# Optimization experiments

Hardware: AMD Instinct MI355X
Metric: run time of the kernel (lower is better)

Reference implementation:

```python
import jax, jax.numpy as jnp
import numpy as np

N_NODES = 50000
N_EDGES = 300000
H = 256
LN_EPS = 1e-5
NEG_SLOPE = 0.2  # PyG GATConv default


def layer_norm(x, g, b):
    mu = x.mean(-1, keepdims=True)
    var = ((x - mu) ** 2).mean(-1, keepdims=True)
    return (x - mu) * jax.lax.rsqrt(var + LN_EPS) * g + b


def gat_conv(x, src, dst, mask, W, a_src, a_dst, bias):
    # PyG GATConv(heads=1, concat=False) on the edge subset selected by `mask`,
    # with self-loops added for every node (PyG default add_self_loops=True).
    N = x.shape[0]
    h = x @ W                              # [N,H]
    s = h @ a_src                          # [N] alpha_src per node
    d = h @ a_dst                          # [N] alpha_dst per node
    e = jax.nn.leaky_relu(s[src] + d[dst], NEG_SLOPE)    # [E]
    e_masked = jnp.where(mask, e, -1e30)
    e_self = jax.nn.leaky_relu(s + d, NEG_SLOPE)         # [N] self-loop logits
    m = jnp.maximum(jax.ops.segment_max(e_masked, dst, num_segments=N), e_self)
    w = jnp.where(mask, jnp.exp(e - m[dst]), 0.0)        # masked edges -> 0
    w_self = jnp.exp(e_self - m)
    denom = jax.ops.segment_sum(w, dst, num_segments=N) + w_self
    num = jax.ops.segment_sum(w[:, None] * h[src], dst, num_segments=N) + w_self[:, None] * h
    return num / denom[:, None] + bias


def setup_inputs() -> dict:
    key = jax.random.key(0)
    ks = jax.random.split(key, 20)
    sc = 1.0 / np.sqrt(H)
    inp = {
        "x": jax.random.normal(ks[0], (N_NODES, H), jnp.float32),
        "edge_index": jax.random.randint(ks[1], (2, N_EDGES), 0, N_NODES, jnp.int64),
        "edge_attr": jax.random.randint(ks[2], (N_EDGES,), 0, 4, jnp.int64),
        # per-branch GATConv params (branches 0..2)
        "Wg": jax.random.normal(ks[3], (3, H, H), jnp.float32) * sc,
        "a_src": jax.random.normal(ks[4], (3, H), jnp.float32) * sc,
        "a_dst": jax.random.normal(ks[5], (3, H), jnp.float32) * sc,
        "bg": jnp.zeros((3, H), jnp.float32),
        # per-branch slice-strategy MLP: Linear + LayerNorm (+ReLU)
        "Ws": jax.random.normal(ks[6], (4, H, H), jnp.float32) * sc,
        "bs": jnp.zeros((4, H), jnp.float32),
        "gs": jnp.ones((4, H), jnp.float32),
        "betas": jnp.zeros((4, H), jnp.float32),
        # strategy selector MLP
        "W1": jax.random.normal(ks[7], (H, H // 2), jnp.float32) * sc,
        "b1": jnp.zeros((H // 2,), jnp.float32),
        "W2": jax.random.normal(ks[8], (H // 2, 4), jnp.float32) * (1.0 / np.sqrt(H // 2)),
        "b2": jnp.zeros((4,), jnp.float32),
        # fusion block
        "Wf": jax.random.normal(ks[9], (H, H), jnp.float32) * sc,
        "bf": jnp.zeros((H,), jnp.float32),
        "gf": jnp.ones((H,), jnp.float32),
        "betaf": jnp.zeros((H,), jnp.float32),
    }
    return inp


def reference(x, edge_index, edge_attr, Wg, a_src, a_dst, bg, Ws, bs, gs, betas,
              W1, b1, W2, b2, Wf, bf, gf, betaf):
    # strategy weights from mean graph representation (eval mode: dropout = identity)
    g = x.mean(axis=0)
    sw = jax.nn.softmax(jax.nn.relu(g @ W1 + b1) @ W2 + b2)  # [4]
    src, dst = edge_index[0], edge_index[1]
    combined = jnp.zeros_like(x)
    for i in range(4):
        if i < 3:
            xi = gat_conv(x, src, dst, edge_attr == i, Wg[i], a_src[i], a_dst[i], bg[i])
        else:
            xi = x
        si = jax.nn.relu(layer_norm(xi @ Ws[i] + bs[i], gs[i], betas[i]))
        combined = combined + si * sw[i]
    return jax.nn.relu(layer_norm(combined @ Wf + bf, gf, betaf))
```

## Files before the change

### kernel.cpp

```cpp
#include <hip/hip_runtime.h>

typedef unsigned short u16;
typedef short s16x8 __attribute__((ext_vector_type(8)));
typedef float f32x4 __attribute__((ext_vector_type(4)));
typedef u16 u16x4 __attribute__((ext_vector_type(4)));

#define NN 50000
#define NE 300000
#define HH 256
#define NCHUNK 196
#define NRC 98
#define NPB 12500

__device__ __forceinline__ float b2f(u16 u) {
  union { float f; unsigned int i; } v; v.i = ((unsigned int)u) << 16; return v.f;
}
__device__ __forceinline__ u16 f2b(float f) {
  union { float f; unsigned int i; } v; v.f = f;
  unsigned int u = v.i;
  unsigned int r = (u + 0x7fffu + ((u >> 16) & 1u)) >> 16;
  return (u16)r;
}
__device__ __forceinline__ float lrelu(float x) { return x > 0.f ? x : 0.2f * x; }

#define GLOAD_LDS16(SRC, DST)                                                   \
  __builtin_amdgcn_global_load_lds(                                             \
      (const __attribute__((address_space(1))) void*)(SRC),                     \
      (__attribute__((address_space(3))) void*)(DST), 16, 0, 0)

__device__ __forceinline__ f32x4 MFMA(s16x8 a, s16x8 b, f32x4 c) {
  return __builtin_amdgcn_mfma_f32_16x16x32_bf16(a, b, c, 0, 0, 0);
}

__device__ __forceinline__ void stageBhalf(const u16* __restrict__ BT, int half,
                                           char* lds, int lane, int wid) {
#pragma unroll
  for (int j = 0; j < 16; ++j) {
    int idx = j * 4 + wid;
    int q = idx >> 4, rem = idx & 15;
    int nf = rem >> 1, ks = rem & 1;
    int col = half * 128 + (lane & 15) + 16 * nf;
    GLOAD_LDS16((const char*)BT + col * 512 + q * 128 + ks * 64 + (lane >> 4) * 16,
                lds + idx * 1024);
  }
}

#define SGEMM_TILE(APTR, ASTRIDE, ACOLOFF)                                      \
  f32x4 acc[2][8] = {};                                                         \
  {                                                                             \
    s16x8 a[2][8];                                                              \
    const u16* a0p = (APTR) + (size_t)ar0 * (ASTRIDE) + (ACOLOFF) + cq8;        \
    const u16* a1p = (APTR) + (size_t)ar1 * (ASTRIDE) + (ACOLOFF) + cq8;        \
    _Pragma("unroll")                                                           \
    for (int ksp = 0; ksp < 8; ++ksp) {                                         \
      a[0][ksp] = *(const s16x8*)(a0p + ksp * 32);                              \
      a[1][ksp] = *(const s16x8*)(a1p + ksp * 32);                              \
    }                                                                           \
    _Pragma("unroll")                                                           \
    for (int ksp = 0; ksp < 8; ++ksp) {                                         \
      const char* bb = lds + (ksp >> 1) * 16384 + (ksp & 1) * 1024 + lane * 16; \
      _Pragma("unroll")                                                         \
      for (int nf = 0; nf < 8; ++nf) {                                          \
        s16x8 bf = *(const s16x8*)(bb + nf * 2048);                             \
        acc[0][nf] = MFMA(a[0][ksp], bf, acc[0][nf]);                           \
        acc[1][nf] = MFMA(a[1][ksp], bf, acc[1][nf]);                           \
      }                                                                         \
    }                                                                           \
  }

__global__ __launch_bounds__(256) void hgemm_s(
    const u16* __restrict__ xb, const u16* __restrict__ WT,
    const float* __restrict__ asrc, const float* __restrict__ adst,
    u16* __restrict__ h768, float* __restrict__ pSd, float* __restrict__ pDd,
    int M) {
  __shared__ __align__(16) char lds[65536];
  int cid = blockIdx.x;
  int rem = cid % 6, chunk = cid / 6;
  int b = rem >> 1, half = rem & 1;
  int tid = threadIdx.x, lane = tid & 63, wid = tid >> 6;
  int colL = lane & 15, cq = lane >> 4, cq8 = cq * 8;

  stageBhalf(WT + (size_t)b * 65536, half, lds, lane, wid);

  float a4[8], dd4[8];
#pragma unroll
  for (int nf = 0; nf < 8; ++nf) {
    int c = half * 128 + colL + nf * 16;
    a4[nf] = asrc[b * 256 + c];
    dd4[nf] = adst[b * 256 + c];
  }
  float* st1 = pSd + (size_t)(b * 2 + half) * NN;
  float* st2 = pDd + (size_t)(b * 2 + half) * NN;
  __syncthreads();

  for (int rt = 0; rt < 4; ++rt) {
    int rowbase = chunk * 512 + rt * 128 + wid * 32;
    if (rowbase >= M) break;
    int ar0 = rowbase + colL; if (ar0 > M - 1) ar0 = M - 1;
    int ar1 = ar0 + 16; if (ar1 > M - 1) ar1 = M - 1;
    SGEMM_TILE(xb, 256, 0)
#pragma unroll
    for (int i = 0; i < 2; ++i)
#pragma unroll
      for (int r = 0; r < 4; ++r) {
        float sp = 0.f, dp = 0.f;
#pragma unroll
        for (int nf = 0; nf < 8; ++nf) {
          float v = acc[i][nf][r];
          sp += v * a4[nf]; dp += v * dd4[nf];
        }
#pragma unroll
        for (int m = 1; m < 16; m <<= 1) { sp += __shfl_xor(sp, m); dp += __shfl_xor(dp, m); }
        int row = rowbase + i * 16 + cq * 4 + r;
        if (row < M) {
          if (colL == 0) { st1[row] = sp; st2[row] = dp; }
          u16* orow = h768 + (size_t)row * 768 + b * 256 + half * 128 + colL;
#pragma unroll
          for (int nf = 0; nf < 8; ++nf) orow[nf * 16] = f2b(acc[i][nf][r]);
        }
      }
  }
}

__global__ __launch_bounds__(256) void wsgemm_s(
    const u16* __restrict__ xiall, const u16* __restrict__ xb,
    const u16* __restrict__ WT, const float* __restrict__ bs,
    u16* __restrict__ y_raw, float* __restrict__ pS, float* __restrict__ pQ,
    int M) {
  __shared__ __align__(16) char lds[65536];
  int cid = blockIdx.x;
  int rem = cid & 7, chunk = cid >> 3;
  int b = rem >> 1, half = rem & 1;
  int tid = threadIdx.x, lane = tid & 63, wid = tid >> 6;
  int colL = lane & 15, cq = lane >> 4, cq8 = cq * 8;

  const u16* Ap = (b < 3) ? xiall : xb;
  int strideA = (b < 3) ? 768 : 256;
  int coloffA = (b < 3) ? b * 256 : 0;

  stageBhalf(WT + (size_t)(3 + b) * 65536, half, lds, lane, wid);

  float bv[8];
#pragma unroll
  for (int nf = 0; nf < 8; ++nf)
    bv[nf] = bs[b * 256 + half * 128 + colL + nf * 16];
  float* st1 = pS + (size_t)(b * 2 + half) * NN;
  float* st2 = pQ + (size_t)(b * 2 + half) * NN;
  u16* yb = y_raw + (size_t)b * NN * 256;
  __syncthreads();

  for (int rt = 0; rt < 4; ++rt) {
    int rowbase = chunk * 512 + rt * 128 + wid * 32;
    if (rowbase >= M) break;
    int ar0 = rowbase + colL; if (ar0 > M - 1) ar0 = M - 1;
    int ar1 = ar0 + 16; if (ar1 > M - 1) ar1 = M - 1;
    SGEMM_TILE(Ap, strideA, coloffA)
#pragma unroll
    for (int i = 0; i < 2; ++i)
#pragma unroll
      for (int r = 0; r < 4; ++r) {
        float s = 0.f, q = 0.f;
#pragma unroll
        for (int nf = 0; nf < 8; ++nf) {
          float v = acc[i][nf][r] + bv[nf];
          acc[i][nf][r] = v;
          s += v; q += v * v;
        }
#pragma unroll
        for (int m = 1; m < 16; m <<= 1) { s += __shfl_xor(s, m); q += __shfl_xor(q, m); }
        int row = rowbase + i * 16 + cq * 4 + r;
        if (row < M) {
          if (colL == 0) { st1[row] = s; st2[row] = q; }
          u16* orow = yb + (size_t)row * 256 + half * 128 + colL;
#pragma unroll
          for (int nf = 0; nf < 8; ++nf) orow[nf * 16] = f2b(acc[i][nf][r]);
        }
      }
  }
}

__global__ __launch_bounds__(256) void fingemm_s(
    const u16* __restrict__ comb, const u16* __restrict__ WT7,
    const float* __restrict__ bfv, u16* __restrict__ z_raw,
    float* __restrict__ pFS, float* __restrict__ pFQ, int M) {
  __shared__ __align__(16) char lds[65536];
  int cid = blockIdx.x;
  int half = cid & 1, chunk = cid >> 1;
  int tid = threadIdx.x, lane = tid & 63, wid = tid >> 6;
  int colL = lane & 15, cq = lane >> 4, cq8 = cq * 8;

  stageBhalf(WT7, half, lds, lane, wid);

  float bv[8];
#pragma unroll
  for (int nf = 0; nf < 8; ++nf)
    bv[nf] = bfv[half * 128 + colL + nf * 16];
  float* st1 = pFS + (size_t)half * NN;
  float* st2 = pFQ + (size_t)half * NN;
  __syncthreads();

  for (int rt = 0; rt < 4; ++rt) {
    int rowbase = chunk * 512 + rt * 128 + wid * 32;
    if (rowbase >= M) break;
    int ar0 = rowbase + colL; if (ar0 > M - 1) ar0 = M - 1;
    int ar1 = ar0 + 16; if (ar1 > M - 1) ar1 = M - 1;
    SGEMM_TILE(comb, 256, 0)
#pragma unroll
    for (int i = 0; i < 2; ++i)
#pragma unroll
      for (int r = 0; r < 4; ++r) {
        float s = 0.f, q = 0.f;
#pragma unroll
        for (int nf = 0; nf < 8; ++nf) {
          float v = acc[i][nf][r] + bv[nf];
          acc[i][nf][r] = v;
          s += v; q += v * v;
        }
#pragma unroll
        for (int m = 1; m < 16; m <<= 1) { s += __shfl_xor(s, m); q += __shfl_xor(q, m); }
        int row = rowbase + i * 16 + cq * 4 + r;
        if (row < M) {
          if (colL == 0) { st1[row] = s; st2[row] = q; }
          u16* orow = z_raw + (size_t)row * 256 + half * 128 + colL;
#pragma unroll
          for (int nf = 0; nf < 8; ++nf) orow[nf * 16] = f2b(acc[i][nf][r]);
        }
      }
  }
}

__global__ void sdfix(const float* __restrict__ pSd, const float* __restrict__ pDd,
                      float* __restrict__ s_arr, float* __restrict__ d_arr) {
  int i = blockIdx.x * 256 + threadIdx.x;
  if (i >= 3 * NN) return;
  int b = i / NN, v = i - b * NN;
  s_arr[i] = pSd[(size_t)(2 * b) * NN + v] + pSd[(size_t)(2 * b + 1) * NN + v];
  d_arr[i] = pDd[(size_t)(2 * b) * NN + v] + pDd[(size_t)(2 * b + 1) * NN + v];
}

__global__ void ln4(const u16* __restrict__ y_raw, const float* __restrict__ pS,
                    const float* __restrict__ pQ, const float* __restrict__ gs,
                    const float* __restrict__ betas, const float* __restrict__ sw,
                    u16* __restrict__ comb) {
  int v = blockIdx.x * 4 + (threadIdx.x >> 6);
  int lane = threadIdx.x & 63;
  int c0 = lane * 4;
  float accv[4] = {0.f, 0.f, 0.f, 0.f};
#pragma unroll
  for (int b = 0; b < 4; ++b) {
    float s = pS[(size_t)(2 * b) * NN + v] + pS[(size_t)(2 * b + 1) * NN + v];
    float q = pQ[(size_t)(2 * b) * NN + v] + pQ[(size_t)(2 * b + 1) * NN + v];
    float mu = s * (1.0f / HH);
    float var = q * (1.0f / HH) - mu * mu;
    float rs = rsqrtf(var + 1e-5f);
    float w = sw[b];
    u16x4 yv = *(const u16x4*)(y_raw + ((size_t)b * NN + v) * 256 + c0);
#pragma unroll
    for (int k = 0; k < 4; ++k) {
      float t = (b2f(yv[k]) - mu) * rs * gs[b * 256 + c0 + k] + betas[b * 256 + c0 + k];
      accv[k] += w * (t > 0.f ? t : 0.f);
    }
  }
  u16x4 o;
#pragma unroll
  for (int k = 0; k < 4; ++k) o[k] = f2b(accv[k]);
  *(u16x4*)(comb + (size_t)v * 256 + c0) = o;
}

__global__ void lnout(const u16* __restrict__ z_raw, const float* __restrict__ pFS,
                      const float* __restrict__ pFQ, const float* __restrict__ gf,
                      const float* __restrict__ betaf, float* __restrict__ outf) {
  int v = blockIdx.x * 4 + (threadIdx.x >> 6);
  int lane = threadIdx.x & 63;
  int c0 = lane * 4;
  float s = pFS[v] + pFS[(size_t)NN + v];
  float q = pFQ[v] + pFQ[(size_t)NN + v];
  float mu = s * (1.0f / HH);
  float var = q * (1.0f / HH) - mu * mu;
  float rs = rsqrtf(var + 1e-5f);
  u16x4 zv = *(const u16x4*)(z_raw + (size_t)v * 256 + c0);
  f32x4 o;
#pragma unroll
  for (int k = 0; k < 4; ++k) {
    float t = (b2f(zv[k]) - mu) * rs * gf[c0 + k] + betaf[c0 + k];
    o[k] = t > 0.f ? t : 0.f;
  }
  *(f32x4*)(outf + (size_t)v * 256 + c0) = o;
}

__global__ void xprep2(const float* __restrict__ x, u16* __restrict__ xb,
                       float* __restrict__ pg) {
  int tid = threadIdx.x, lane = tid & 63, w = tid >> 6;
  int r = blockIdx.x * 4 + w;
  f32x4 v = *(const f32x4*)(x + (size_t)r * HH + lane * 4);
  u16x4 o;
#pragma unroll
  for (int k = 0; k < 4; ++k) o[k] = f2b(v[k]);
  *(u16x4*)(xb + (size_t)r * HH + lane * 4) = o;
  __shared__ f32x4 sh[256];
  sh[tid] = v;
  __syncthreads();
  if (tid < 64) {
    f32x4 t = sh[tid] + sh[tid + 64] + sh[tid + 128] + sh[tid + 192];
    *(f32x4*)(pg + (size_t)blockIdx.x * 256 + lane * 4) = t;
  }
}

__global__ void gsum_red(const float* __restrict__ pg, float* __restrict__ g_sum) {
  int t = threadIdx.x;
  int r0 = blockIdx.x * 98;
  float s = 0.f;
  for (int r = r0; r < r0 + 98 && r < NPB; ++r) s += pg[(size_t)r * 256 + t];
  atomicAdd(&g_sum[t], s);
}

__global__ void transpose_all(const float* __restrict__ Wg, const float* __restrict__ Wsm,
                              const float* __restrict__ Wf, u16* __restrict__ WT) {
  __shared__ float tile[32][33];
  int z = blockIdx.z;
  const float* src = (z < 3) ? (Wg + (size_t)z * 65536)
                   : (z < 7) ? (Wsm + (size_t)(z - 3) * 65536) : Wf;
  u16* dst = WT + (size_t)z * 65536;
  int tx = threadIdx.x, ty = threadIdx.y;
  int bx = blockIdx.x, by = blockIdx.y;
#pragma unroll
  for (int j = 0; j < 32; j += 8)
    tile[ty + j][tx] = src[(size_t)(by * 32 + ty + j) * 256 + bx * 32 + tx];
  __syncthreads();
#pragma unroll
  for (int j = 0; j < 32; j += 8)
    dst[(size_t)(bx * 32 + ty + j) * 256 + by * 32 + tx] = f2b(tile[tx][ty + j]);
}

__global__ void selector_kernel(const float* __restrict__ g_sum,
                                const float* __restrict__ W1, const float* __restrict__ b1,
                                const float* __restrict__ W2, const float* __restrict__ b2,
                                float* __restrict__ sw) {
  __shared__ float gg[256];
  __shared__ float hid[128];
  __shared__ float lg[4];
  int t = threadIdx.x;
  gg[t] = g_sum[t] * (1.0f / NN);
  gg[t + 128] = g_sum[t + 128] * (1.0f / NN);
  __syncthreads();
  float a = 0.f;
  for (int c = 0; c < 256; ++c) a += gg[c] * W1[c * 128 + t];
  a += b1[t];
  hid[t] = a > 0.f ? a : 0.f;
  __syncthreads();
  if (t < 4) {
    float s = 0.f;
    for (int j = 0; j < 128; ++j) s += hid[j] * W2[j * 4 + t];
    lg[t] = s + b2[t];
  }
  __syncthreads();
  if (t == 0) {
    float m = fmaxf(fmaxf(lg[0], lg[1]), fmaxf(lg[2], lg[3]));
    float e0 = __expf(lg[0] - m), e1 = __expf(lg[1] - m);
    float e2 = __expf(lg[2] - m), e3 = __expf(lg[3] - m);
    float inv = 1.0f / (e0 + e1 + e2 + e3);
    sw[0] = e0 * inv; sw[1] = e1 * inv; sw[2] = e2 * inv; sw[3] = e3 * inv;
  }
}

__global__ void detect_kernel(const int* __restrict__ ei_raw, int* __restrict__ flag) {
  int t = threadIdx.x;
  int nz = 0;
  for (int k = t; k < 1024; k += 256) nz |= (ei_raw[2 * k + 1] != 0);
  if (nz) atomicOr(flag, 1);
}

__global__ void norm_edges(const int* __restrict__ ei_raw, const int* __restrict__ ea_raw,
                           const int* __restrict__ flag, int* __restrict__ srcE,
                           int* __restrict__ dstE, int* __restrict__ attrE) {
  int e = blockIdx.x * 256 + threadIdx.x;
  if (e >= NE) return;
  if (*flag) {
    srcE[e] = ei_raw[e];
    dstE[e] = ei_raw[NE + e];
    attrE[e] = ea_raw[e];
  } else {
    srcE[e] = ei_raw[2 * e];
    dstE[e] = ei_raw[2 * NE + 2 * e];
    attrE[e] = ea_raw[2 * e];
  }
}

__global__ void hist_kernel(const int* __restrict__ dstE, const int* __restrict__ attrE,
                            int* __restrict__ counts) {
  int e = blockIdx.x * 256 + threadIdx.x;
  if (e < NE) {
    int a = attrE[e];
    if ((unsigned)a < 3u) atomicAdd(&counts[a * NN + dstE[e]], 1);
  }
}

__global__ void scan1(const int* __restrict__ counts, int* __restrict__ offs,
                      int* __restrict__ bsum) {
  int b = blockIdx.y, c = blockIdx.x, t = threadIdx.x;
  int idx = c * 256 + t;
  int v = (idx < NN) ? counts[b * NN + idx] : 0;
  __shared__ int sh[256];
  sh[t] = v;
  __syncthreads();
  for (int o = 1; o < 256; o <<= 1) {
    int add = (t >= o) ? sh[t - o] : 0;
    __syncthreads();
    sh[t] += add;
    __syncthreads();
  }
  int incl = sh[t];
  if (idx < NN) offs[b * (NN + 1) + idx] = incl - v;
  if (t == 255) bsum[b * NCHUNK + c] = incl;
}

__global__ void scan2(const int* __restrict__ bsum, int* __restrict__ bpre,
                      int* __restrict__ offs) {
  int t = threadIdx.x;
  if (t < 3) {
    int run = 0;
    for (int c = 0; c < NCHUNK; ++c) { bpre[t * NCHUNK + c] = run; run += bsum[t * NCHUNK + c]; }
    offs[t * (NN + 1) + NN] = run;
  }
}

__global__ void scan3(const int* __restrict__ bpre, int* __restrict__ offs,
                      int* __restrict__ cur) {
  int b = blockIdx.y, c = blockIdx.x;
  int idx = c * 256 + threadIdx.x;
  if (idx < NN) {
    int val = offs[b * (NN + 1) + idx] + bpre[b * NCHUNK + c];
    offs[b * (NN + 1) + idx] = val;
    cur[b * NN + idx] = val;
  }
}

__global__ void scatter_kernel(const int* __restrict__ srcE, const int* __restrict__ dstE,
                               const int* __restrict__ attrE, int* __restrict__ cur,
                               int* __restrict__ elist) {
  int e = blockIdx.x * 256 + threadIdx.x;
  if (e < NE) {
    int a = attrE[e];
    if ((unsigned)a < 3u) {
      int p = atomicAdd(&cur[a * NN + dstE[e]], 1);
      elist[a * NE + p] = srcE[e];
    }
  }
}

__global__ void gat3(const int* __restrict__ offs, const int* __restrict__ elist,
                     const float* __restrict__ s_all, const float* __restrict__ d_all,
                     const u16* __restrict__ h, const float* __restrict__ bg,
                     u16* __restrict__ xiall) {
  int b = blockIdx.y;
  const int* offs_b = offs + (size_t)b * (NN + 1);
  const int* elist_b = elist + (size_t)b * NE;
  const float* s = s_all + (size_t)b * NN;
  const float* d = d_all + (size_t)b * NN;
  const float* bgrow = bg + b * 256;
  int v = blockIdx.x * 4 + (threadIdx.x >> 6);
  int lane = threadIdx.x & 63;
  float dv = d[v], sv = s[v];
  float eself = lrelu(sv + dv);
  int beg = offs_b[v], end = offs_b[v + 1];
  float m = eself;
  for (int j = beg; j < end; ++j) m = fmaxf(m, lrelu(s[elist_b[j]] + dv));
  float denom = 0.f;
  float acc[4] = {0.f, 0.f, 0.f, 0.f};
  for (int j = beg; j < end; ++j) {
    int u = elist_b[j];
    float w = __expf(lrelu(s[u] + dv) - m);
    denom += w;
    u16x4 hv = *(const u16x4*)(h + (size_t)u * 768 + b * 256 + lane * 4);
#pragma unroll
    for (int k = 0; k < 4; ++k) acc[k] += w * b2f(hv[k]);
  }
  float wself = __expf(eself - m);
  denom += wself;
  u16x4 hv = *(const u16x4*)(h + (size_t)v * 768 + b * 256 + lane * 4);
#pragma unroll
  for (int k = 0; k < 4; ++k) acc[k] += wself * b2f(hv[k]);
  float inv = 1.0f / denom;
  f32x4 bg4 = *(const f32x4*)(bgrow + lane * 4);
  u16x4 outv;
#pragma unroll
  for (int k = 0; k < 4; ++k) outv[k] = f2b(acc[k] * inv + bg4[k]);
  *(u16x4*)(xiall + (size_t)v * 768 + b * 256 + lane * 4) = outv;
}

extern "C" void kernel_launch(void* const* d_in, const int* in_sizes, int n_in,
                              void* d_out, int out_size, void* d_ws, size_t ws_size,
                              hipStream_t stream) {
  const float* x   = (const float*)d_in[0];
  const int* ei    = (const int*)d_in[1];
  const int* ea    = (const int*)d_in[2];
  const float* Wg  = (const float*)d_in[3];
  const float* asrc= (const float*)d_in[4];
  const float* adst= (const float*)d_in[5];
  const float* bg  = (const float*)d_in[6];
  const float* Wsm = (const float*)d_in[7];
  const float* bs  = (const float*)d_in[8];
  const float* gs  = (const float*)d_in[9];
  const float* betas=(const float*)d_in[10];
  const float* W1  = (const float*)d_in[11];
  const float* b1  = (const float*)d_in[12];
  const float* W2  = (const float*)d_in[13];
  const float* b2  = (const float*)d_in[14];
  const float* Wf  = (const float*)d_in[15];
  const float* bfv = (const float*)d_in[16];
  const float* gf  = (const float*)d_in[17];
  const float* betaf=(const float*)d_in[18];
  float* out = (float*)d_out;

  char* wsb = (char*)d_ws;
  size_t off = 0;
  auto alloc = [&](size_t bytes) -> void* {
    void* p = wsb + off;
    off += bytes;
    off = (off + 255) & ~(size_t)255;
    return p;
  };
  int* flag    = (int*)alloc(sizeof(int));
  float* g_sum = (float*)alloc(256 * sizeof(float));
  float* sw    = (float*)alloc(4 * sizeof(float));
  int* counts  = (int*)alloc((size_t)3 * NN * sizeof(int));
  int* offs    = (int*)alloc((size_t)3 * (NN + 1) * sizeof(int));
  int* cur     = (int*)alloc((size_t)3 * NN * sizeof(int));
  int* bsum    = (int*)alloc((size_t)3 * NCHUNK * sizeof(int));
  int* bpre    = (int*)alloc((size_t)3 * NCHUNK * sizeof(int));
  int* srcE    = (int*)alloc((size_t)NE * sizeof(int));
  int* dstE    = (int*)alloc((size_t)NE * sizeof(int));
  int* attrE   = (int*)alloc((size_t)NE * sizeof(int));
  int* elist   = (int*)alloc((size_t)3 * NE * sizeof(int));
  float* s_arr = (float*)alloc((size_t)3 * NN * sizeof(float));
  float* d_arr = (float*)alloc((size_t)3 * NN * sizeof(float));
  float* pSd   = (float*)alloc((size_t)6 * NN * sizeof(float));
  float* pDd   = (float*)alloc((size_t)6 * NN * sizeof(float));
  float* pS    = (float*)alloc((size_t)8 * NN * sizeof(float));
  float* pQ    = (float*)alloc((size_t)8 * NN * sizeof(float));
  float* pFS   = (float*)alloc((size_t)2 * NN * sizeof(float));
  float* pFQ   = (float*)alloc((size_t)2 * NN * sizeof(float));
  float* pg    = (float*)alloc((size_t)NPB * 256 * sizeof(float));
  u16* WT      = (u16*)alloc((size_t)8 * 65536 * sizeof(u16));
  u16* xb      = (u16*)alloc((size_t)NN * HH * sizeof(u16));
  u16* h768    = (u16*)alloc((size_t)NN * 768 * sizeof(u16));
  u16* yb3     = (u16*)alloc((size_t)NN * 256 * sizeof(u16));
  u16* xiall   = (u16*)alloc((size_t)NN * 768 * sizeof(u16));
  u16* y_raw   = h768;
  u16* comb    = xiall;
  u16* z_raw   = xiall + (size_t)NN * 256;
  (void)yb3; (void)ws_size; (void)in_sizes; (void)n_in; (void)out_size;

  hipMemsetAsync(flag, 0, sizeof(int), stream);
  hipMemsetAsync(g_sum, 0, 256 * sizeof(float), stream);
  hipMemsetAsync(counts, 0, (size_t)3 * NN * sizeof(int), stream);

  detect_kernel<<<1, 256, 0, stream>>>(ei, flag);
  norm_edges<<<(NE + 255) / 256, 256, 0, stream>>>(ei, ea, flag, srcE, dstE, attrE);

  transpose_all<<<dim3(8, 8, 8), dim3(32, 8), 0, stream>>>(Wg, Wsm, Wf, WT);
  xprep2<<<NPB, 256, 0, stream>>>(x, xb, pg);
  gsum_red<<<128, 256, 0, stream>>>(pg, g_sum);
  selector_kernel<<<1, 128, 0, stream>>>(g_sum, W1, b1, W2, b2, sw);

  hist_kernel<<<(NE + 255) / 256, 256, 0, stream>>>(dstE, attrE, counts);
  scan1<<<dim3(NCHUNK, 3), 256, 0, stream>>>(counts, offs, bsum);
  scan2<<<1, 64, 0, stream>>>(bsum, bpre, offs);
  scan3<<<dim3(NCHUNK, 3), 256, 0, stream>>>(bpre, offs, cur);
  scatter_kernel<<<(NE + 255) / 256, 256, 0, stream>>>(srcE, dstE, attrE, cur, elist);

  hgemm_s<<<6 * NRC, 256, 0, stream>>>(xb, WT, asrc, adst, h768, pSd, pDd, NN);
  sdfix<<<(3 * NN + 255) / 256, 256, 0, stream>>>(pSd, pDd, s_arr, d_arr);
  gat3<<<dim3(12500, 3), 256, 0, stream>>>(offs, elist, s_arr, d_arr, h768, bg, xiall);
  wsgemm_s<<<8 * NRC, 256, 0, stream>>>(xiall, xb, WT, bs, y_raw, pS, pQ, NN);
  ln4<<<12500, 256, 0, stream>>>(y_raw, pS, pQ, gs, betas, sw, comb);
  fingemm_s<<<2 * NRC, 256, 0, stream>>>(comb, WT + (size_t)7 * 65536, bfv, z_raw, pFS, pFQ, NN);
  lnout<<<12500, 256, 0, stream>>>(z_raw, pFS, pFQ, gf, betaf, out);
}
```

Measured before the change: 373.3 us.

## Split GEMM columns into quarter tiles and stage epilogue stores through LDS

Each of the three GEMM kernels now handles a 64-column quarter of the weight matrix instead of a 128-column half, which doubles the block count and halves the accumulator registers per thread. The epilogue now writes bf16 results into a per-wave LDS buffer and reads them back as 16-byte rows, replacing scattered 2-byte global stores. The goal is more parallelism and occupancy plus coalesced output writes. In exchange, every A row is loaded twice as often across blocks, two barriers are added per row tile, and the partial-statistic arrays double in size.

```diff
diff --git a/kernel.cpp b/kernel.cpp
--- a/kernel.cpp
+++ b/kernel.cpp
@@ -11,6 +11,7 @@
 #define NCHUNK 196
 #define NRC 98
 #define NPB 12500
+#define BNC 17408
 
 __device__ __forceinline__ float b2f(u16 u) {
   union { float f; unsigned int i; } v; v.i = ((unsigned int)u) << 16; return v.f;
@@ -32,21 +33,21 @@
   return __builtin_amdgcn_mfma_f32_16x16x32_bf16(a, b, c, 0, 0, 0);
 }
 
-__device__ __forceinline__ void stageBhalf(const u16* __restrict__ BT, int half,
-                                           char* lds, int lane, int wid) {
-#pragma unroll
-  for (int j = 0; j < 16; ++j) {
+__device__ __forceinline__ void stageBq(const u16* __restrict__ BT, int qt,
+                                        char* lds, int lane, int wid) {
+#pragma unroll
+  for (int j = 0; j < 8; ++j) {
     int idx = j * 4 + wid;
-    int q = idx >> 4, rem = idx & 15;
+    int q = idx >> 3, rem = idx & 7;
     int nf = rem >> 1, ks = rem & 1;
-    int col = half * 128 + (lane & 15) + 16 * nf;
+    int col = qt * 64 + (lane & 15) + 16 * nf;
     GLOAD_LDS16((const char*)BT + col * 512 + q * 128 + ks * 64 + (lane >> 4) * 16,
                 lds + idx * 1024);
   }
 }
 
 #define SGEMM_TILE(APTR, ASTRIDE, ACOLOFF)                                      \
-  f32x4 acc[2][8] = {};                                                         \
+  f32x4 acc[2][4] = {};                                                         \
   {                                                                             \
     s16x8 a[2][8];                                                              \
     const u16* a0p = (APTR) + (size_t)ar0 * (ASTRIDE) + (ACOLOFF) + cq8;        \
@@ -58,9 +59,9 @@
     }                                                                           \
     _Pragma("unroll")                                                           \
     for (int ksp = 0; ksp < 8; ++ksp) {                                         \
-      const char* bb = lds + (ksp >> 1) * 16384 + (ksp & 1) * 1024 + lane * 16; \
+      const char* bb = lds + (ksp >> 1) * 8192 + (ksp & 1) * 1024 + lane * 16;  \
       _Pragma("unroll")                                                         \
-      for (int nf = 0; nf < 8; ++nf) {                                          \
+      for (int nf = 0; nf < 4; ++nf) {                                          \
         s16x8 bf = *(const s16x8*)(bb + nf * 2048);                             \
         acc[0][nf] = MFMA(a[0][ksp], bf, acc[0][nf]);                           \
         acc[1][nf] = MFMA(a[1][ksp], bf, acc[1][nf]);                           \
@@ -68,29 +69,55 @@
     }                                                                           \
   }
 
+#define EPI_STORE(OUTBASE, OSTRIDE_BYTES, OCOLOFF_BYTES)                        \
+  {                                                                             \
+    char* bw = bnc + wid * BNC;                                                 \
+    _Pragma("unroll")                                                           \
+    for (int i = 0; i < 2; ++i)                                                 \
+      _Pragma("unroll")                                                         \
+      for (int r = 0; r < 4; ++r) {                                             \
+        int lrow = i * 16 + cq * 4 + r;                                         \
+        _Pragma("unroll")                                                       \
+        for (int nf = 0; nf < 4; ++nf)                                          \
+          *(u16*)(bw + lrow * 136 + (colL + nf * 16) * 2) = f2b(acc[i][nf][r]); \
+      }                                                                         \
+    __syncthreads();                                                            \
+    _Pragma("unroll")                                                           \
+    for (int t = 0; t < 4; ++t) {                                               \
+      int row8 = t * 8 + (lane >> 3);                                           \
+      int row = rowbase + row8;                                                 \
+      s16x8 vv = *(const s16x8*)(bw + row8 * 136 + (lane & 7) * 16);            \
+      if (row < M)                                                              \
+        *(s16x8*)((char*)(OUTBASE) + (size_t)row * (OSTRIDE_BYTES) +            \
+                  (OCOLOFF_BYTES) + (lane & 7) * 16) = vv;                      \
+    }                                                                           \
+    __syncthreads();                                                            \
+  }
+
 __global__ __launch_bounds__(256) void hgemm_s(
     const u16* __restrict__ xb, const u16* __restrict__ WT,
     const float* __restrict__ asrc, const float* __restrict__ adst,
     u16* __restrict__ h768, float* __restrict__ pSd, float* __restrict__ pDd,
     int M) {
-  __shared__ __align__(16) char lds[65536];
+  __shared__ __align__(16) char lds[32768 + 4 * BNC];
+  char* bnc = lds + 32768;
   int cid = blockIdx.x;
-  int rem = cid % 6, chunk = cid / 6;
-  int b = rem >> 1, half = rem & 1;
+  int rem = cid % 12, chunk = cid / 12;
+  int b = rem >> 2, qt = rem & 3;
   int tid = threadIdx.x, lane = tid & 63, wid = tid >> 6;
   int colL = lane & 15, cq = lane >> 4, cq8 = cq * 8;
 
-  stageBhalf(WT + (size_t)b * 65536, half, lds, lane, wid);
-
-  float a4[8], dd4[8];
-#pragma unroll
-  for (int nf = 0; nf < 8; ++nf) {
-    int c = half * 128 + colL + nf * 16;
+  stageBq(WT + (size_t)b * 65536, qt, lds, lane, wid);
+
+  float a4[4], dd4[4];
+#pragma unroll
+  for (int nf = 0; nf < 4; ++nf) {
+    int c = qt * 64 + colL + nf * 16;
     a4[nf] = asrc[b * 256 + c];
     dd4[nf] = adst[b * 256 + c];
   }
-  float* st1 = pSd + (size_t)(b * 2 + half) * NN;
-  float* st2 = pDd + (size_t)(b * 2 + half) * NN;
+  float* st1 = pSd + (size_t)(b * 4 + qt) * NN;
+  float* st2 = pDd + (size_t)(b * 4 + qt) * NN;
   __syncthreads();
 
   for (int rt = 0; rt < 4; ++rt) {
@@ -105,20 +132,16 @@
       for (int r = 0; r < 4; ++r) {
         float sp = 0.f, dp = 0.f;
 #pragma unroll
-        for (int nf = 0; nf < 8; ++nf) {
+        for (int nf = 0; nf < 4; ++nf) {
           float v = acc[i][nf][r];
           sp += v * a4[nf]; dp += v * dd4[nf];
         }
 #pragma unroll
         for (int m = 1; m < 16; m <<= 1) { sp += __shfl_xor(sp, m); dp += __shfl_xor(dp, m); }
         int row = rowbase + i * 16 + cq * 4 + r;
-        if (row < M) {
-          if (colL == 0) { st1[row] = sp; st2[row] = dp; }
-          u16* orow = h768 + (size_t)row * 768 + b * 256 + half * 128 + colL;
-#pragma unroll
-          for (int nf = 0; nf < 8; ++nf) orow[nf * 16] = f2b(acc[i][nf][r]);
-        }
+        if (colL == 0 && row < M) { st1[row] = sp; st2[row] = dp; }
       }
+    EPI_STORE(h768, 1536, b * 512 + qt * 128)
   }
 }
 
@@ -127,10 +150,11 @@
     const u16* __restrict__ WT, const float* __restrict__ bs,
     u16* __restrict__ y_raw, float* __restrict__ pS, float* __restrict__ pQ,
     int M) {
-  __shared__ __align__(16) char lds[65536];
+  __shared__ __align__(16) char lds[32768 + 4 * BNC];
+  char* bnc = lds + 32768;
   int cid = blockIdx.x;
-  int rem = cid & 7, chunk = cid >> 3;
-  int b = rem >> 1, half = rem & 1;
+  int rem = cid & 15, chunk = cid >> 4;
+  int b = rem >> 2, qt = rem & 3;
   int tid = threadIdx.x, lane = tid & 63, wid = tid >> 6;
   int colL = lane & 15, cq = lane >> 4, cq8 = cq * 8;
 
@@ -138,14 +162,14 @@
   int strideA = (b < 3) ? 768 : 256;
   int coloffA = (b < 3) ? b * 256 : 0;
 
-  stageBhalf(WT + (size_t)(3 + b) * 65536, half, lds, lane, wid);
-
-  float bv[8];
-#pragma unroll
-  for (int nf = 0; nf < 8; ++nf)
-    bv[nf] = bs[b * 256 + half * 128 + colL + nf * 16];
-  float* st1 = pS + (size_t)(b * 2 + half) * NN;
-  float* st2 = pQ + (size_t)(b * 2 + half) * NN;
+  stageBq(WT + (size_t)(3 + b) * 65536, qt, lds, lane, wid);
+
+  float bv[4];
+#pragma unroll
+  for (int nf = 0; nf < 4; ++nf)
+    bv[nf] = bs[b * 256 + qt * 64 + colL + nf * 16];
+  float* st1 = pS + (size_t)(b * 4 + qt) * NN;
+  float* st2 = pQ + (size_t)(b * 4 + qt) * NN;
   u16* yb = y_raw + (size_t)b * NN * 256;
   __syncthreads();
 
@@ -161,7 +185,7 @@
       for (int r = 0; r < 4; ++r) {
         float s = 0.f, q = 0.f;
 #pragma unroll
-        for (int nf = 0; nf < 8; ++nf) {
+        for (int nf = 0; nf < 4; ++nf) {
           float v = acc[i][nf][r] + bv[nf];
           acc[i][nf][r] = v;
           s += v; q += v * v;
@@ -169,13 +193,9 @@
 #pragma unroll
         for (int m = 1; m < 16; m <<= 1) { s += __shfl_xor(s, m); q += __shfl_xor(q, m); }
         int row = rowbase + i * 16 + cq * 4 + r;
-        if (row < M) {
-          if (colL == 0) { st1[row] = s; st2[row] = q; }
-          u16* orow = yb + (size_t)row * 256 + half * 128 + colL;
-#pragma unroll
-          for (int nf = 0; nf < 8; ++nf) orow[nf * 16] = f2b(acc[i][nf][r]);
-        }
+        if (colL == 0 && row < M) { st1[row] = s; st2[row] = q; }
       }
+    EPI_STORE(yb, 512, qt * 128)
   }
 }
 
@@ -183,20 +203,21 @@
     const u16* __restrict__ comb, const u16* __restrict__ WT7,
     const float* __restrict__ bfv, u16* __restrict__ z_raw,
     float* __restrict__ pFS, float* __restrict__ pFQ, int M) {
-  __shared__ __align__(16) char lds[65536];
+  __shared__ __align__(16) char lds[32768 + 4 * BNC];
+  char* bnc = lds + 32768;
   int cid = blockIdx.x;
-  int half = cid & 1, chunk = cid >> 1;
+  int qt = cid & 3, chunk = cid >> 2;
   int tid = threadIdx.x, lane = tid & 63, wid = tid >> 6;
   int colL = lane & 15, cq = lane >> 4, cq8 = cq * 8;
 
-  stageBhalf(WT7, half, lds, lane, wid);
-
-  float bv[8];
-#pragma unroll
-  for (int nf = 0; nf < 8; ++nf)
-    bv[nf] = bfv[half * 128 + colL + nf * 16];
-  float* st1 = pFS + (size_t)half * NN;
-  float* st2 = pFQ + (size_t)half * NN;
+  stageBq(WT7, qt, lds, lane, wid);
+
+  float bv[4];
+#pragma unroll
+  for (int nf = 0; nf < 4; ++nf)
+    bv[nf] = bfv[qt * 64 + colL + nf * 16];
+  float* st1 = pFS + (size_t)qt * NN;
+  float* st2 = pFQ + (size_t)qt * NN;
   __syncthreads();
 
   for (int rt = 0; rt < 4; ++rt) {
@@ -211,7 +232,7 @@
       for (int r = 0; r < 4; ++r) {
         float s = 0.f, q = 0.f;
 #pragma unroll
-        for (int nf = 0; nf < 8; ++nf) {
+        for (int nf = 0; nf < 4; ++nf) {
           float v = acc[i][nf][r] + bv[nf];
           acc[i][nf][r] = v;
           s += v; q += v * v;
@@ -219,13 +240,9 @@
 #pragma unroll
         for (int m = 1; m < 16; m <<= 1) { s += __shfl_xor(s, m); q += __shfl_xor(q, m); }
         int row = rowbase + i * 16 + cq * 4 + r;
-        if (row < M) {
-          if (colL == 0) { st1[row] = s; st2[row] = q; }
-          u16* orow = z_raw + (size_t)row * 256 + half * 128 + colL;
-#pragma unroll
-          for (int nf = 0; nf < 8; ++nf) orow[nf * 16] = f2b(acc[i][nf][r]);
-        }
+        if (colL == 0 && row < M) { st1[row] = s; st2[row] = q; }
       }
+    EPI_STORE(z_raw, 512, qt * 128)
   }
 }
 
@@ -234,8 +251,13 @@
   int i = blockIdx.x * 256 + threadIdx.x;
   if (i >= 3 * NN) return;
   int b = i / NN, v = i - b * NN;
-  s_arr[i] = pSd[(size_t)(2 * b) * NN + v] + pSd[(size_t)(2 * b + 1) * NN + v];
-  d_arr[i] = pDd[(size_t)(2 * b) * NN + v] + pDd[(size_t)(2 * b + 1) * NN + v];
+  float s = 0.f, d = 0.f;
+#pragma unroll
+  for (int qt = 0; qt < 4; ++qt) {
+    s += pSd[(size_t)(4 * b + qt) * NN + v];
+    d += pDd[(size_t)(4 * b + qt) * NN + v];
+  }
+  s_arr[i] = s; d_arr[i] = d;
 }
 
 __global__ void ln4(const u16* __restrict__ y_raw, const float* __restrict__ pS,
@@ -248,8 +270,12 @@
   float accv[4] = {0.f, 0.f, 0.f, 0.f};
 #pragma unroll
   for (int b = 0; b < 4; ++b) {
-    float s = pS[(size_t)(2 * b) * NN + v] + pS[(size_t)(2 * b + 1) * NN + v];
-    float q = pQ[(size_t)(2 * b) * NN + v] + pQ[(size_t)(2 * b + 1) * NN + v];
+    float s = 0.f, q = 0.f;
+#pragma unroll
+    for (int qt = 0; qt < 4; ++qt) {
+      s += pS[(size_t)(4 * b + qt) * NN + v];
+      q += pQ[(size_t)(4 * b + qt) * NN + v];
+    }
     float mu = s * (1.0f / HH);
     float var = q * (1.0f / HH) - mu * mu;
     float rs = rsqrtf(var + 1e-5f);
@@ -273,8 +299,12 @@
   int v = blockIdx.x * 4 + (threadIdx.x >> 6);
   int lane = threadIdx.x & 63;
   int c0 = lane * 4;
-  float s = pFS[v] + pFS[(size_t)NN + v];
-  float q = pFQ[v] + pFQ[(size_t)NN + v];
+  float s = 0.f, q = 0.f;
+#pragma unroll
+  for (int qt = 0; qt < 4; ++qt) {
+    s += pFS[(size_t)qt * NN + v];
+    q += pFQ[(size_t)qt * NN + v];
+  }
   float mu = s * (1.0f / HH);
   float var = q * (1.0f / HH) - mu * mu;
   float rs = rsqrtf(var + 1e-5f);
@@ -534,12 +564,12 @@
   int* elist   = (int*)alloc((size_t)3 * NE * sizeof(int));
   float* s_arr = (float*)alloc((size_t)3 * NN * sizeof(float));
   float* d_arr = (float*)alloc((size_t)3 * NN * sizeof(float));
-  float* pSd   = (float*)alloc((size_t)6 * NN * sizeof(float));
-  float* pDd   = (float*)alloc((size_t)6 * NN * sizeof(float));
-  float* pS    = (float*)alloc((size_t)8 * NN * sizeof(float));
-  float* pQ    = (float*)alloc((size_t)8 * NN * sizeof(float));
-  float* pFS   = (float*)alloc((size_t)2 * NN * sizeof(float));
-  float* pFQ   = (float*)alloc((size_t)2 * NN * sizeof(float));
+  float* pSd   = (float*)alloc((size_t)12 * NN * sizeof(float));
+  float* pDd   = (float*)alloc((size_t)12 * NN * sizeof(float));
+  float* pS    = (float*)alloc((size_t)16 * NN * sizeof(float));
+  float* pQ    = (float*)alloc((size_t)16 * NN * sizeof(float));
+  float* pFS   = (float*)alloc((size_t)4 * NN * sizeof(float));
+  float* pFQ   = (float*)alloc((size_t)4 * NN * sizeof(float));
   float* pg    = (float*)alloc((size_t)NPB * 256 * sizeof(float));
   u16* WT      = (u16*)alloc((size_t)8 * 65536 * sizeof(u16));
   u16* xb      = (u16*)alloc((size_t)NN * HH * sizeof(u16));
@@ -569,11 +599,11 @@
   scan3<<<dim3(NCHUNK, 3), 256, 0, stream>>>(bpre, offs, cur);
   scatter_kernel<<<(NE + 255) / 256, 256, 0, stream>>>(srcE, dstE, attrE, cur, elist);
 
-  hgemm_s<<<6 * NRC, 256, 0, stream>>>(xb, WT, asrc, adst, h768, pSd, pDd, NN);
+  hgemm_s<<<12 * NRC, 256, 0, stream>>>(xb, WT, asrc, adst, h768, pSd, pDd, NN);
   sdfix<<<(3 * NN + 255) / 256, 256, 0, stream>>>(pSd, pDd, s_arr, d_arr);
   gat3<<<dim3(12500, 3), 256, 0, stream>>>(offs, elist, s_arr, d_arr, h768, bg, xiall);
-  wsgemm_s<<<8 * NRC, 256, 0, stream>>>(xiall, xb, WT, bs, y_raw, pS, pQ, NN);
+  wsgemm_s<<<16 * NRC, 256, 0, stream>>>(xiall, xb, WT, bs, y_raw, pS, pQ, NN);
   ln4<<<12500, 256, 0, stream>>>(y_raw, pS, pQ, gs, betas, sw, comb);
-  fingemm_s<<<2 * NRC, 256, 0, stream>>>(comb, WT + (size_t)7 * 65536, bfv, z_raw, pFS, pFQ, NN);
+  fingemm_s<<<4 * NRC, 256, 0, stream>>>(comb, WT + (size_t)7 * 65536, bfv, z_raw, pFS, pFQ, NN);
   lnout<<<12500, 256, 0, stream>>>(z_raw, pFS, pFQ, gf, betaf, out);
 }
```

After: 530.7 us. 1.42x slower.
